# Kernel tuning notes

Measured on AMD Instinct MI355X. Metric: run time of the kernel, lower is better.

## Reference

```python
import jax, jax.numpy as jnp
import numpy as np

B = 64          # batch
C = 80          # num_classes
IN_CH = 300     # word-embedding channel
J = 8192        # JOINT_EMB_SIZE (linear_intermediate)
S = 8           # pooling_stride
OUT = J // S    # out_in_tmp = 1024


def setup_inputs() -> dict:
    key = jax.random.key(0)
    ks = jax.random.split(key, 8)
    w = lambda k, sh: jax.random.normal(k, sh, jnp.float32) * 0.02
    return {
        "feature": jax.random.normal(ks[0], (B, 2048, 14, 14), jnp.float32),
        "inp": jax.random.normal(ks[1], (1, C, IN_CH), jnp.float32),
        "A": jax.random.uniform(ks[2], (C, C), jnp.float32),  # positive co-occurrence adjacency
        "W_gc1": w(ks[3], (IN_CH, 1024)),
        "W_gc2": w(ks[4], (1024, 2048)),
        "W_img": w(ks[5], (J, 2048)),
        "b_img": jnp.zeros((J,), jnp.float32),
        "W_cls": w(ks[6], (J, 2048)),
        "b_cls": jnp.zeros((J,), jnp.float32),
        "W_ml": w(ks[7], (C, C * OUT)),
        "b_ml": jnp.zeros((C,), jnp.float32),
    }


def reference(feature, inp, A, W_gc1, W_gc2, W_img, b_img, W_cls, b_cls, W_ml, b_ml):
    # backbone output -> MaxPool2d(14,14) over a 14x14 map == global spatial max
    feat = feature.max(axis=(2, 3))                       # [B, 2048]

    # gen_adj(A).detach(): D = diag(rowsum(A)^-0.5); adj = D @ A.T @ D
    dinv = jnp.sum(A, axis=1) ** -0.5                     # [C]
    adj = jax.lax.stop_gradient(A.T * dinv[:, None] * dinv[None, :])  # [C, C]

    # two GCN layers on label embeddings
    x = adj @ (inp[0] @ W_gc1)                            # [C, 1024]
    x = jax.nn.leaky_relu(x, 0.2)
    x = adj @ (x @ W_gc2)                                 # [C, 2048]

    # MFB bilinear fusion (vectorized form of the nested batch/class loops;
    # dropout is identity in eval mode)
    img = feat @ W_img.T + b_img                          # [B, J]
    cls = x @ W_cls.T + b_cls                             # [C, J]
    # sum-pool over the stride axis of the elementwise product:
    # iq[b,c,o] = sum_s img[b,o*S+s] * cls[c,o*S+s]
    pooled = jnp.einsum('bos,cos->bco',
                        img.reshape(B, OUT, S),
                        cls.reshape(C, OUT, S))           # [B, C, OUT]
    # torch.cat order over class columns -> c-major flatten, then ML_fc_layer
    out = pooled.reshape(B, C * OUT) @ W_ml.T + b_ml      # [B, C]
    return out
```

## Files before the change

kernel.cpp:

```cpp
#include <hip/hip_runtime.h>
#include <hip/hip_bf16.h>
#include <cstdint>
#include <cstddef>

typedef float  f32x4  __attribute__((ext_vector_type(4)));
typedef __bf16 bf16x8 __attribute__((ext_vector_type(8)));
typedef unsigned short u16x8 __attribute__((ext_vector_type(8)));

__device__ __forceinline__ unsigned short f2bf(float f) {
    unsigned u = __float_as_uint(f);
    u += 0x7FFFu + ((u >> 16) & 1u);
    return (unsigned short)(u >> 16);
}


constexpr size_t OFF_FEATB = 0;
constexpr size_t OFF_ADJ   = 262144;
constexpr size_t OFF_Y0    = 287744;
constexpr size_t OFF_X1    = 615424;
constexpr size_t OFF_X2B   = 943104;
constexpr size_t OFF_WG2T  = 1106944;
constexpr size_t OFF_XB    = 9495552;
constexpr size_t OFF_IMG   = 9823232;
constexpr size_t OFF_CLS   = 11920384;
constexpr size_t OFF_G     = 14541824;


__device__ __forceinline__ void maxpool_role(int base_row, int bid,
                                             const float* __restrict__ feature,
                                             unsigned short* __restrict__ featb) {
    int wave = threadIdx.x >> 6, lane = threadIdx.x & 63;
    int r = lane >> 4, q = lane & 15;
    #pragma unroll
    for (int it = 0; it < 4; ++it) {
        int row = base_row + bid * 128 + it * 32 + wave * 4 + r;
        const float4* p = (const float4*)(feature + (size_t)row * 196);
        float4 a = p[q], b = p[q + 16], c = p[q + 32];
        float m = fmaxf(fmaxf(fmaxf(a.x, a.y), fmaxf(a.z, a.w)),
                 fmaxf(fmaxf(fmaxf(b.x, b.y), fmaxf(b.z, b.w)),
                       fmaxf(fmaxf(c.x, c.y), fmaxf(c.z, c.w))));
        if (q == 0) {
            float4 d = p[48];
            m = fmaxf(m, fmaxf(fmaxf(d.x, d.y), fmaxf(d.z, d.w)));
        }
        #pragma unroll
        for (int off = 1; off < 16; off <<= 1) m = fmaxf(m, __shfl_xor(m, off));
        if (q == 0) featb[row] = f2bf(m);
    }
}

template <int KS>
__device__ __forceinline__ void skinny_role(int idx, const float* __restrict__ X,
                                            const float* __restrict__ W,
                                            float* __restrict__ outf,
                                            unsigned short* __restrict__ outb,
                                            int leaky, float4* red ) {
    int c = idx >> 1, jh = idx & 1;
    int t = threadIdx.x;
    int jq = t & 127, ks = t >> 7;
    int j = jh * 512 + jq * 4;
    const float* xr = X + c * 4 * KS + ks * KS;
    const float* wp = W + (size_t)(ks * KS) * 1024 + j;
    float4 acc = {0.f, 0.f, 0.f, 0.f};
    #pragma unroll 5
    for (int k = 0; k < KS; k++) {
        float a = xr[k];
        float4 w = *(const float4*)(wp + (size_t)k * 1024);
        acc.x = fmaf(a, w.x, acc.x);
        acc.y = fmaf(a, w.y, acc.y);
        acc.z = fmaf(a, w.z, acc.z);
        acc.w = fmaf(a, w.w, acc.w);
    }
    red[ks * 128 + jq] = acc;
    __syncthreads();
    if (ks == 0) {
        float4 s0 = red[jq], s1 = red[128 + jq], s2 = red[256 + jq], s3 = red[384 + jq];
        float4 s;
        s.x = s0.x + s1.x + s2.x + s3.x;
        s.y = s0.y + s1.y + s2.y + s3.y;
        s.z = s0.z + s1.z + s2.z + s3.z;
        s.w = s0.w + s1.w + s2.w + s3.w;
        if (leaky) {
            if (s.x < 0.f) s.x *= 0.2f;
            if (s.y < 0.f) s.y *= 0.2f;
            if (s.z < 0.f) s.z *= 0.2f;
            if (s.w < 0.f) s.w *= 0.2f;
        }
        size_t o = (size_t)c * 1024 + j;
        if (outf) *(float4*)(outf + o) = s;
        if (outb) {
            unsigned short b4[4] = {f2bf(s.x), f2bf(s.y), f2bf(s.z), f2bf(s.w)};
            *(uint64_t*)(outb + o) = *(const uint64_t*)b4;
        }
    }
}

__device__ __forceinline__ void transpose_role(int idx, const float* __restrict__ in,
                                               float* __restrict__ out, float* t ) {
    int c0 = (idx & 31) * 64, r0 = (idx >> 5) * 64;
    int tx = threadIdx.x & 63, ty = threadIdx.x >> 6;
    #pragma unroll
    for (int i = 0; i < 64; i += 8)
        t[(ty + i) * 65 + tx] = in[(size_t)(r0 + ty + i) * 2048 + c0 + tx];
    __syncthreads();
    #pragma unroll
    for (int i = 0; i < 64; i += 8)
        out[(size_t)(c0 + ty + i) * 1024 + r0 + tx] = t[tx * 65 + (ty + i)];
}

__device__ __forceinline__ void adj_role(const float* __restrict__ A, float* __restrict__ adjp,
                                         float* dinv ) {
    int t = threadIdx.x;
    if (t < 80) {
        const float4* ar = (const float4*)(A + t * 80);
        float4 s4 = {0.f, 0.f, 0.f, 0.f};
        #pragma unroll
        for (int j = 0; j < 20; j++) {
            float4 v = ar[j];
            s4.x += v.x; s4.y += v.y; s4.z += v.z; s4.w += v.w;
        }
        dinv[t] = 1.0f / sqrtf(s4.x + s4.y + s4.z + s4.w);
    }
    __syncthreads();
    for (int i = t; i < 6400; i += 512) {
        int r = i / 80, cc = i % 80;
        adjp[i] = A[cc * 80 + r] * dinv[r] * dinv[cc];
    }
}

template <int MF>
__device__ __forceinline__ void gemm_block(int bx, const unsigned short* __restrict__ X,
                                           const float* __restrict__ W,
                                           const float* __restrict__ bias,
                                           float* __restrict__ outf,
                                           unsigned short* __restrict__ outb,
                                           int N, int K, float (*red)[64][21]) {
    int tid = threadIdx.x;
    int wave = tid >> 6, lane = tid & 63;
    int nf = wave & 1, ks = wave >> 1;
    int n = bx * 32 + nf * 16 + (lane & 15);
    int rowa = lane & 15;
    int koff = (lane >> 4) * 8;
    int Kc = K >> 2;
    int k0 = ks * Kc;

    f32x4 acc[MF];
    #pragma unroll
    for (int i = 0; i < MF; i++) acc[i] = (f32x4)(0.f);

    const float* wrow = W + (size_t)n * K;

    #pragma unroll 2
    for (int k = k0; k < k0 + Kc; k += 32) {
        float4 w0 = *(const float4*)(wrow + k + koff);
        float4 w1 = *(const float4*)(wrow + k + koff + 4);
        u16x8 bu;
        bu[0] = f2bf(w0.x); bu[1] = f2bf(w0.y); bu[2] = f2bf(w0.z); bu[3] = f2bf(w0.w);
        bu[4] = f2bf(w1.x); bu[5] = f2bf(w1.y); bu[6] = f2bf(w1.z); bu[7] = f2bf(w1.w);
        bf16x8 bf = __builtin_bit_cast(bf16x8, bu);
        #pragma unroll
        for (int mf = 0; mf < MF; mf++) {
            u16x8 au = *(const u16x8*)(X + (size_t)(mf * 16 + rowa) * K + k + koff);
            acc[mf] = __builtin_amdgcn_mfma_f32_16x16x32_bf16(
                __builtin_bit_cast(bf16x8, au), bf, acc[mf], 0, 0, 0);
        }
    }

    #pragma unroll
    for (int mf = 0; mf < MF; mf++)
        #pragma unroll
        for (int i = 0; i < 4; i++)
            red[wave][lane][mf * 4 + i] = acc[mf][i];
    __syncthreads();

    int lane2 = tid & 63, sg = (tid >> 6) & 3, nf2 = tid >> 8;
    int n2 = bx * 32 + nf2 * 16 + (lane2 & 15);
    float b = bias ? bias[n2] : 0.f;
    #pragma unroll
    for (int mf = 0; mf < MF; mf++) {
        int slot = mf * 4 + sg;
        float s = red[0 + nf2][lane2][slot] + red[2 + nf2][lane2][slot]
                + red[4 + nf2][lane2][slot] + red[6 + nf2][lane2][slot] + b;
        int row = mf * 16 + (lane2 >> 4) * 4 + sg;
        size_t o = (size_t)row * N + n2;
        if (outf) outf[o] = s;
        if (outb) outb[o] = f2bf(s);
    }
}


__global__ __launch_bounds__(512, 4) void kA(const float* __restrict__ inp,
                                             const float* __restrict__ W1,
                                             float* __restrict__ y0,
                                             const float* __restrict__ A,
                                             float* __restrict__ adjp,
                                             const float* __restrict__ Wg2,
                                             float* __restrict__ wg2t,
                                             const float* __restrict__ feature,
                                             unsigned short* __restrict__ featb) {
    __shared__ __align__(16) float lds[64 * 65];
    int b = blockIdx.x;
    if (b < 160)       skinny_role<75>(b, inp, W1, y0, nullptr, 0, (float4*)lds);
    else if (b < 161)  adj_role(A, adjp, lds);
    else if (b < 673)  transpose_role(b - 161, Wg2, wg2t, lds);
    else               maxpool_role(0, b - 673, feature, featb);
}

__global__ __launch_bounds__(512, 4) void kB(const float* __restrict__ adjp,
                                             const float* __restrict__ y0,
                                             float* __restrict__ x1,
                                             const float* __restrict__ feature,
                                             unsigned short* __restrict__ featb) {
    __shared__ __align__(16) float4 red[512];
    int b = blockIdx.x;
    if (b < 160) skinny_role<20>(b, adjp, y0, x1, nullptr, 1, red);
    else         maxpool_role(32768, b - 160, feature, featb);
}

__global__ __launch_bounds__(512, 4) void kC(const float* __restrict__ adjp,
                                             const float* __restrict__ x1,
                                             unsigned short* __restrict__ x2b,
                                             const float* __restrict__ feature,
                                             unsigned short* __restrict__ featb) {
    __shared__ __align__(16) float4 red[512];
    int b = blockIdx.x;
    if (b < 160) skinny_role<20>(b, adjp, x1, nullptr, x2b, 0, red);
    else         maxpool_role(65536, b - 160, feature, featb);
}

__global__ __launch_bounds__(512, 4) void kD(const unsigned short* __restrict__ x2b,
                                             const float* __restrict__ wg2t,
                                             unsigned short* __restrict__ xb,
                                             const float* __restrict__ feature,
                                             unsigned short* __restrict__ featb) {
    __shared__ __align__(16) float red[8][64][21];
    int b = blockIdx.x;
    if (b < 64) gemm_block<5>(b, x2b, wg2t, nullptr, nullptr, xb, 2048, 1024, red);
    else        maxpool_role(98304, b - 64, feature, featb);
}

__global__ __launch_bounds__(512, 4) void kE(const unsigned short* __restrict__ xb,
                                             const float* __restrict__ W_cls,
                                             const float* __restrict__ b_cls,
                                             float* __restrict__ cls) {
    __shared__ __align__(16) float red[8][64][21];
    gemm_block<5>(blockIdx.x, xb, W_cls, b_cls, cls, nullptr, 8192, 2048, red);
}

__global__ __launch_bounds__(512, 2) void kF(const unsigned short* __restrict__ featb,
                                             const float* __restrict__ W_img,
                                             const float* __restrict__ b_img,
                                             float* __restrict__ img,
                                             const float* __restrict__ cls,
                                             const float* __restrict__ W_ml,
                                             float* __restrict__ G) {
    __shared__ __align__(16) float smem[20480];
    int b = blockIdx.x;
    if (b < 256) {
        gemm_block<4>(b, featb, W_img, b_img, img, nullptr, 8192, 2048,
                      (float (*)[64][21])smem);
    } else {
        float (*wml)[80][16] = (float (*)[80][16])smem;
        int idx = b - 256;
        int o0 = (idx & 63) * 16;
        int c2b = (idx >> 6) * 16;
        int j0 = o0 * 8;
        for (int i = threadIdx.x; i < 16 * 80 * 16; i += 512) {
            int ol = i & 15, c = (i >> 4) % 80, c2 = i / 1280;
            wml[c2][c][ol] = W_ml[(size_t)(c2b + c2) * 81920 + c * 1024 + o0 + ol];
        }
        __syncthreads();
        int jl = threadIdx.x & 127;
        int c2l = (threadIdx.x >> 7) * 4;
        int ol = jl >> 3;
        float acc[4] = {0.f, 0.f, 0.f, 0.f};
        for (int c = 0; c < 80; c++) {
            float cv = cls[(size_t)c * 8192 + j0 + jl];
            #pragma unroll
            for (int i = 0; i < 4; i++) acc[i] = fmaf(cv, wml[c2l + i][c][ol], acc[i]);
        }
        #pragma unroll
        for (int i = 0; i < 4; i++) G[(size_t)(c2b + c2l + i) * 8192 + j0 + jl] = acc[i];
    }
}

__global__ __launch_bounds__(512, 4) void kG(const float* __restrict__ img,
                                             const float* __restrict__ G,
                                             const float* __restrict__ b_ml,
                                             float* __restrict__ out) {
    __shared__ float sm[8][32];
    int btile = blockIdx.x, cg = blockIdx.y;
    int kc = threadIdx.x >> 6, lane = threadIdx.x & 63;
    float acc[4][8];
    #pragma unroll
    for (int q = 0; q < 4; q++)
        #pragma unroll
        for (int i = 0; i < 8; i++) acc[q][i] = 0.f;

    #pragma unroll
    for (int step = 0; step < 4; step++) {
        int k = kc * 1024 + step * 256 + lane * 4;
        float4 gv[8];
        #pragma unroll
        for (int i = 0; i < 8; i++) gv[i] = *(const float4*)(G + (size_t)(cg * 8 + i) * 8192 + k);
        #pragma unroll
        for (int q = 0; q < 4; q++) {
            float4 iv = *(const float4*)(img + (size_t)(btile * 4 + q) * 8192 + k);
            #pragma unroll
            for (int i = 0; i < 8; i++) {
                acc[q][i] = fmaf(iv.x, gv[i].x, acc[q][i]);
                acc[q][i] = fmaf(iv.y, gv[i].y, acc[q][i]);
                acc[q][i] = fmaf(iv.z, gv[i].z, acc[q][i]);
                acc[q][i] = fmaf(iv.w, gv[i].w, acc[q][i]);
            }
        }
    }
    #pragma unroll
    for (int q = 0; q < 4; q++)
        #pragma unroll
        for (int i = 0; i < 8; i++) {
            float v = acc[q][i];
            #pragma unroll
            for (int off = 32; off; off >>= 1) v += __shfl_xor(v, off);
            if (lane == 0) sm[kc][q * 8 + i] = v;
        }
    __syncthreads();
    if (threadIdx.x < 32) {
        int i = threadIdx.x & 7;
        float s = b_ml[cg * 8 + i];
        #pragma unroll
        for (int kk = 0; kk < 8; kk++) s += sm[kk][threadIdx.x];
        int q = threadIdx.x >> 3;
        out[(size_t)(btile * 4 + q) * 80 + cg * 8 + i] = s;
    }
}

extern "C" void kernel_launch(void* const* d_in, const int* in_sizes, int n_in,
                              void* d_out, int out_size, void* d_ws, size_t ws_size,
                              hipStream_t stream) {
    (void)in_sizes; (void)n_in; (void)out_size; (void)ws_size;
    const float* feature = (const float*)d_in[0];
    const float* inp     = (const float*)d_in[1];
    const float* A       = (const float*)d_in[2];
    const float* W_gc1   = (const float*)d_in[3];
    const float* W_gc2   = (const float*)d_in[4];
    const float* W_img   = (const float*)d_in[5];
    const float* b_img   = (const float*)d_in[6];
    const float* W_cls   = (const float*)d_in[7];
    const float* b_cls   = (const float*)d_in[8];
    const float* W_ml    = (const float*)d_in[9];
    const float* b_ml    = (const float*)d_in[10];
    float* out = (float*)d_out;
    char*  ws  = (char*)d_ws;

    unsigned short* featb = (unsigned short*)(ws + OFF_FEATB);
    float* adjp = (float*)(ws + OFF_ADJ);
    float* y0   = (float*)(ws + OFF_Y0);
    float* x1   = (float*)(ws + OFF_X1);
    unsigned short* x2b = (unsigned short*)(ws + OFF_X2B);
    float* wg2t = (float*)(ws + OFF_WG2T);
    unsigned short* xb  = (unsigned short*)(ws + OFF_XB);
    float* img  = (float*)(ws + OFF_IMG);
    float* cls  = (float*)(ws + OFF_CLS);
    float* G    = (float*)(ws + OFF_G);

    kA<<<929, 512, 0, stream>>>(inp, W_gc1, y0, A, adjp, W_gc2, wg2t, feature, featb);
    kB<<<416, 512, 0, stream>>>(adjp, y0, x1, feature, featb);
    kC<<<416, 512, 0, stream>>>(adjp, x1, x2b, feature, featb);
    kD<<<320, 512, 0, stream>>>(x2b, wg2t, xb, feature, featb);
    kE<<<256, 512, 0, stream>>>(xb, W_cls, b_cls, cls);
    kF<<<576, 512, 0, stream>>>(featb, W_img, b_img, img, cls, W_ml, G);
    kG<<<dim3(16, 10), 512, 0, stream>>>(img, G, b_ml, out);
}
```

Measured before the change: 156.0 us.

## Fuse seven kernels into one persistent megakernel with atomic grid barriers

Replaces the seven separate launches with a single 256-block persistent kernel. Stages are separated by software grid barriers built on an atomic counter, and the counter is reset by a memset before each launch. The W_img GEMM blocks are spread across the GCN stages to fill idle blocks, which changes how work overlaps between stages. This removes launch gaps and per-kernel tail effects. In exchange it depends on all 256 blocks being resident at once, pays for spin-wait barriers, and has less parallelism in stages that used to launch more blocks.

```diff
diff --git a/kernel.cpp b/kernel.cpp
--- a/kernel.cpp
+++ b/kernel.cpp
@@ -24,16 +24,28 @@
 constexpr size_t OFF_IMG   = 9823232;
 constexpr size_t OFF_CLS   = 11920384;
 constexpr size_t OFF_G     = 14541824;
-
-
-__device__ __forceinline__ void maxpool_role(int base_row, int bid,
-                                             const float* __restrict__ feature,
+constexpr size_t OFF_CNT   = 17163264;
+
+__device__ __forceinline__ void grid_barrier(unsigned* cnt, unsigned target) {
+    __syncthreads();
+    if (threadIdx.x == 0) {
+        __threadfence();
+        __hip_atomic_fetch_add(cnt, 1u, __ATOMIC_ACQ_REL, __HIP_MEMORY_SCOPE_AGENT);
+        while (__hip_atomic_load(cnt, __ATOMIC_ACQUIRE, __HIP_MEMORY_SCOPE_AGENT) < target)
+            __builtin_amdgcn_s_sleep(2);
+        __threadfence();
+    }
+    __syncthreads();
+}
+
+
+__device__ __forceinline__ void maxpool_role(int vbid, const float* __restrict__ feature,
                                              unsigned short* __restrict__ featb) {
     int wave = threadIdx.x >> 6, lane = threadIdx.x & 63;
     int r = lane >> 4, q = lane & 15;
     #pragma unroll
     for (int it = 0; it < 4; ++it) {
-        int row = base_row + bid * 128 + it * 32 + wave * 4 + r;
+        int row = vbid * 128 + it * 32 + wave * 4 + r;
         const float4* p = (const float4*)(feature + (size_t)row * 196);
         float4 a = p[q], b = p[q + 16], c = p[q + 32];
         float m = fmaxf(fmaxf(fmaxf(a.x, a.y), fmaxf(a.z, a.w)),
@@ -93,6 +105,7 @@
             *(uint64_t*)(outb + o) = *(const uint64_t*)b4;
         }
     }
+    __syncthreads();
 }
 
 __device__ __forceinline__ void transpose_role(int idx, const float* __restrict__ in,
@@ -166,6 +179,7 @@
         }
     }
 
+    __syncthreads();
     #pragma unroll
     for (int mf = 0; mf < MF; mf++)
         #pragma unroll
@@ -186,110 +200,41 @@
         if (outf) outf[o] = s;
         if (outb) outb[o] = f2bf(s);
     }
-}
-
-
-__global__ __launch_bounds__(512, 4) void kA(const float* __restrict__ inp,
-                                             const float* __restrict__ W1,
-                                             float* __restrict__ y0,
-                                             const float* __restrict__ A,
-                                             float* __restrict__ adjp,
-                                             const float* __restrict__ Wg2,
-                                             float* __restrict__ wg2t,
-                                             const float* __restrict__ feature,
-                                             unsigned short* __restrict__ featb) {
-    __shared__ __align__(16) float lds[64 * 65];
-    int b = blockIdx.x;
-    if (b < 160)       skinny_role<75>(b, inp, W1, y0, nullptr, 0, (float4*)lds);
-    else if (b < 161)  adj_role(A, adjp, lds);
-    else if (b < 673)  transpose_role(b - 161, Wg2, wg2t, lds);
-    else               maxpool_role(0, b - 673, feature, featb);
-}
-
-__global__ __launch_bounds__(512, 4) void kB(const float* __restrict__ adjp,
-                                             const float* __restrict__ y0,
-                                             float* __restrict__ x1,
-                                             const float* __restrict__ feature,
-                                             unsigned short* __restrict__ featb) {
-    __shared__ __align__(16) float4 red[512];
-    int b = blockIdx.x;
-    if (b < 160) skinny_role<20>(b, adjp, y0, x1, nullptr, 1, red);
-    else         maxpool_role(32768, b - 160, feature, featb);
-}
-
-__global__ __launch_bounds__(512, 4) void kC(const float* __restrict__ adjp,
-                                             const float* __restrict__ x1,
-                                             unsigned short* __restrict__ x2b,
-                                             const float* __restrict__ feature,
-                                             unsigned short* __restrict__ featb) {
-    __shared__ __align__(16) float4 red[512];
-    int b = blockIdx.x;
-    if (b < 160) skinny_role<20>(b, adjp, x1, nullptr, x2b, 0, red);
-    else         maxpool_role(65536, b - 160, feature, featb);
-}
-
-__global__ __launch_bounds__(512, 4) void kD(const unsigned short* __restrict__ x2b,
-                                             const float* __restrict__ wg2t,
-                                             unsigned short* __restrict__ xb,
-                                             const float* __restrict__ feature,
-                                             unsigned short* __restrict__ featb) {
-    __shared__ __align__(16) float red[8][64][21];
-    int b = blockIdx.x;
-    if (b < 64) gemm_block<5>(b, x2b, wg2t, nullptr, nullptr, xb, 2048, 1024, red);
-    else        maxpool_role(98304, b - 64, feature, featb);
-}
-
-__global__ __launch_bounds__(512, 4) void kE(const unsigned short* __restrict__ xb,
-                                             const float* __restrict__ W_cls,
-                                             const float* __restrict__ b_cls,
-                                             float* __restrict__ cls) {
-    __shared__ __align__(16) float red[8][64][21];
-    gemm_block<5>(blockIdx.x, xb, W_cls, b_cls, cls, nullptr, 8192, 2048, red);
-}
-
-__global__ __launch_bounds__(512, 2) void kF(const unsigned short* __restrict__ featb,
-                                             const float* __restrict__ W_img,
-                                             const float* __restrict__ b_img,
-                                             float* __restrict__ img,
-                                             const float* __restrict__ cls,
-                                             const float* __restrict__ W_ml,
-                                             float* __restrict__ G) {
-    __shared__ __align__(16) float smem[20480];
-    int b = blockIdx.x;
-    if (b < 256) {
-        gemm_block<4>(b, featb, W_img, b_img, img, nullptr, 8192, 2048,
-                      (float (*)[64][21])smem);
-    } else {
-        float (*wml)[80][16] = (float (*)[80][16])smem;
-        int idx = b - 256;
-        int o0 = (idx & 63) * 16;
-        int c2b = (idx >> 6) * 16;
-        int j0 = o0 * 8;
-        for (int i = threadIdx.x; i < 16 * 80 * 16; i += 512) {
-            int ol = i & 15, c = (i >> 4) % 80, c2 = i / 1280;
-            wml[c2][c][ol] = W_ml[(size_t)(c2b + c2) * 81920 + c * 1024 + o0 + ol];
-        }
-        __syncthreads();
-        int jl = threadIdx.x & 127;
-        int c2l = (threadIdx.x >> 7) * 4;
-        int ol = jl >> 3;
-        float acc[4] = {0.f, 0.f, 0.f, 0.f};
-        for (int c = 0; c < 80; c++) {
-            float cv = cls[(size_t)c * 8192 + j0 + jl];
-            #pragma unroll
-            for (int i = 0; i < 4; i++) acc[i] = fmaf(cv, wml[c2l + i][c][ol], acc[i]);
-        }
-        #pragma unroll
-        for (int i = 0; i < 4; i++) G[(size_t)(c2b + c2l + i) * 8192 + j0 + jl] = acc[i];
-    }
-}
-
-__global__ __launch_bounds__(512, 4) void kG(const float* __restrict__ img,
-                                             const float* __restrict__ G,
-                                             const float* __restrict__ b_ml,
-                                             float* __restrict__ out) {
-    __shared__ float sm[8][32];
-    int btile = blockIdx.x, cg = blockIdx.y;
+    __syncthreads();
+}
+
+__device__ __forceinline__ void g_role(int idx, const float* __restrict__ cls,
+                                       const float* __restrict__ W_ml,
+                                       float* __restrict__ G, float* smem) {
+    float (*wml)[80][16] = (float (*)[80][16])smem;
+    int o0 = (idx & 63) * 16;
+    int c2b = (idx >> 6) * 16;
+    int j0 = o0 * 8;
+    for (int i = threadIdx.x; i < 16 * 80 * 16; i += 512) {
+        int ol = i & 15, c = (i >> 4) % 80, c2 = i / 1280;
+        wml[c2][c][ol] = W_ml[(size_t)(c2b + c2) * 81920 + c * 1024 + o0 + ol];
+    }
+    __syncthreads();
+    int jl = threadIdx.x & 127;
+    int c2l = (threadIdx.x >> 7) * 4;
+    int ol = jl >> 3;
+    float acc[4] = {0.f, 0.f, 0.f, 0.f};
+    for (int c = 0; c < 80; c++) {
+        float cv = cls[(size_t)c * 8192 + j0 + jl];
+        #pragma unroll
+        for (int i = 0; i < 4; i++) acc[i] = fmaf(cv, wml[c2l + i][c][ol], acc[i]);
+    }
+    #pragma unroll
+    for (int i = 0; i < 4; i++) G[(size_t)(c2b + c2l + i) * 8192 + j0 + jl] = acc[i];
+    __syncthreads();
+}
+
+__device__ __forceinline__ void out_role(int unit, const float* __restrict__ img,
+                                         const float* __restrict__ G,
+                                         const float* __restrict__ b_ml,
+                                         float* __restrict__ out, float* smem) {
+    float (*sm)[32] = (float (*)[32])smem;
+    int btile = unit & 15, cg = unit >> 4;
     int kc = threadIdx.x >> 6, lane = threadIdx.x & 63;
     float acc[4][8];
     #pragma unroll
@@ -333,6 +278,60 @@
         int q = threadIdx.x >> 3;
         out[(size_t)(btile * 4 + q) * 80 + cg * 8 + i] = s;
     }
+}
+
+__global__ __launch_bounds__(512, 2) void mega(
+    const float* __restrict__ feature, const float* __restrict__ inp,
+    const float* __restrict__ A,       const float* __restrict__ W_gc1,
+    const float* __restrict__ W_gc2,   const float* __restrict__ W_img,
+    const float* __restrict__ b_img,   const float* __restrict__ W_cls,
+    const float* __restrict__ b_cls,   const float* __restrict__ W_ml,
+    const float* __restrict__ b_ml,
+    unsigned short* featb, float* adjp, float* y0, float* x1,
+    unsigned short* x2b, float* wg2t, unsigned short* xb,
+    float* img, float* cls, float* G, float* out, unsigned* cnt)
+{
+    __shared__ __align__(16) float smem[20480];
+    const int bid = blockIdx.x;
+
+    #pragma unroll
+    for (int it = 0; it < 4; ++it) maxpool_role(bid * 4 + it, feature, featb);
+    for (int tile = 0; tile < 2; ++tile) {
+        __syncthreads();
+        transpose_role(bid * 2 + tile, W_gc2, wg2t, smem);
+    }
+    __syncthreads();
+    if (bid < 160)       skinny_role<75>(bid, inp, W_gc1, y0, nullptr, 0, (float4*)smem);
+    else if (bid == 160) adj_role(A, adjp, smem);
+    grid_barrier(cnt, 256);
+
+    if (bid < 160) skinny_role<20>(bid, adjp, y0, x1, nullptr, 1, (float4*)smem);
+    else gemm_block<4>(bid - 160, featb, W_img, b_img, img, nullptr, 8192, 2048,
+                       (float (*)[64][21])smem);
+    grid_barrier(cnt, 512);
+
+    if (bid < 160) skinny_role<20>(bid, adjp, x1, nullptr, x2b, 0, (float4*)smem);
+    else gemm_block<4>(bid - 160 + 96, featb, W_img, b_img, img, nullptr, 8192, 2048,
+                       (float (*)[64][21])smem);
+    grid_barrier(cnt, 768);
+
+    if (bid < 64)
+        gemm_block<5>(bid, x2b, wg2t, nullptr, nullptr, xb, 2048, 1024,
+                      (float (*)[64][21])smem);
+    else if (bid < 128)
+        gemm_block<4>(bid - 64 + 192, featb, W_img, b_img, img, nullptr, 8192, 2048,
+                      (float (*)[64][21])smem);
+    grid_barrier(cnt, 1024);
+
+    gemm_block<5>(bid, xb, W_cls, b_cls, cls, nullptr, 8192, 2048,
+                  (float (*)[64][21])smem);
+    grid_barrier(cnt, 1280);
+
+    g_role(bid, cls, W_ml, G, smem);
+    if (bid < 64) g_role(256 + bid, cls, W_ml, G, smem);
+    grid_barrier(cnt, 1536);
+
+    if (bid < 160) out_role(bid, img, G, b_ml, out, smem);
 }
 
 extern "C" void kernel_launch(void* const* d_in, const int* in_sizes, int n_in,
@@ -363,12 +362,11 @@
     float* img  = (float*)(ws + OFF_IMG);
     float* cls  = (float*)(ws + OFF_CLS);
     float* G    = (float*)(ws + OFF_G);
-
-    kA<<<929, 512, 0, stream>>>(inp, W_gc1, y0, A, adjp, W_gc2, wg2t, feature, featb);
-    kB<<<416, 512, 0, stream>>>(adjp, y0, x1, feature, featb);
-    kC<<<416, 512, 0, stream>>>(adjp, x1, x2b, feature, featb);
-    kD<<<320, 512, 0, stream>>>(x2b, wg2t, xb, feature, featb);
-    kE<<<256, 512, 0, stream>>>(xb, W_cls, b_cls, cls);
-    kF<<<576, 512, 0, stream>>>(featb, W_img, b_img, img, cls, W_ml, G);
-    kG<<<dim3(16, 10), 512, 0, stream>>>(img, G, b_ml, out);
-}
+    unsigned* cnt = (unsigned*)(ws + OFF_CNT);
+
+    hipMemsetAsync(cnt, 0, 4, stream);
+    mega<<<256, 512, 0, stream>>>(feature, inp, A, W_gc1, W_gc2, W_img, b_img,
+                                  W_cls, b_cls, W_ml, b_ml,
+                                  featb, adjp, y0, x1, x2b, wg2t, xb,
+                                  img, cls, G, out, cnt);
+}
```

Result: slower. 490.2 us (+214.3%).
